# Optimization experiments

Measured on AMD Instinct MI355X. Metric: run time of the kernel, lower is better.

The kernel has to match this reference:

```python
import jax, jax.numpy as jnp
import numpy as np

B, T1, T2 = 2, 1024, 512
D_MODEL, N_HEAD, D_HEAD = 1024, 16, 64
SCALE = 1.0 / D_HEAD ** 0.5
EPS = 1e-5


def _skew(qe):
    # qe: [B, H, T, 2T-1] -> [B, H, T, T] via Transformer-XL pad/reshape trick
    b, h, t, x = qe.shape
    qe = jnp.pad(qe, ((0, 0), (0, 0), (0, 0), (0, 1))).reshape(b, h, 2 * t * t)
    qe = jnp.pad(qe, ((0, 0), (0, 0), (0, t - 1))).reshape(b, h, t + 1, 2 * t - 1)
    return qe[:, :, :t, -t:]


def setup_inputs() -> dict:
    key = jax.random.key(0)
    ks = jax.random.split(key, 12)
    s = 0.02
    return {
        "Q": jax.random.normal(ks[0], (B, T1, D_MODEL), jnp.float32),
        "K": jax.random.normal(ks[1], (B, T1, D_MODEL), jnp.float32),
        "V": jax.random.normal(ks[2], (B, T1, D_MODEL), jnp.float32),
        "lookup_table": jax.random.normal(ks[3], (2 * T1 - 1, D_HEAD), jnp.float32) * s,
        "valid_frames": jnp.sort(jax.random.randint(ks[4], (T2,), 0, T1)),
        "mask": jax.random.bernoulli(ks[5], 0.1, (B, N_HEAD, T1, T2)),
        "Wq": jax.random.normal(ks[6], (D_MODEL, N_HEAD * D_HEAD), jnp.float32) * s,
        "Wk": jax.random.normal(ks[7], (D_MODEL, N_HEAD * D_HEAD), jnp.float32) * s,
        "Wv": jax.random.normal(ks[8], (D_MODEL, N_HEAD * D_HEAD), jnp.float32) * s,
        "Wo": jax.random.normal(ks[9], (N_HEAD * D_HEAD, D_MODEL), jnp.float32) * s,
        "bo": jnp.zeros((D_MODEL,), jnp.float32),
        "ln_g": jnp.ones((D_MODEL,), jnp.float32),
        "ln_b": jnp.zeros((D_MODEL,), jnp.float32),
    }


def reference(Q, K, V, lookup_table, valid_frames, mask, Wq, Wk, Wv, Wo, bo, ln_g, ln_b):
    # gather valid KV frames (raw inputs, before projection)
    K = K[:, valid_frames]  # [B, T2, D]
    V = V[:, valid_frames]
    # pre-layernorm on Q only
    mu = jnp.mean(Q, axis=-1, keepdims=True)
    var = jnp.var(Q, axis=-1, keepdims=True)
    Qn = (Q - mu) * jax.lax.rsqrt(var + EPS) * ln_g + ln_b
    # projections -> [B, H, T, d_head]
    q = (Qn @ Wq).reshape(B, T1, N_HEAD, D_HEAD).transpose(0, 2, 1, 3)
    k = (K @ Wk).reshape(B, T2, N_HEAD, D_HEAD).transpose(0, 2, 1, 3)
    v = (V @ Wv).reshape(B, T2, N_HEAD, D_HEAD).transpose(0, 2, 1, 3)
    # content score + skewed relative-position score
    score = jnp.einsum("bhqd,bhkd->bhqk", q, k)  # [B,H,T1,T2]
    rel = jnp.einsum("bhqd,xd->bhqx", q, lookup_table)  # [B,H,T1,2T1-1]
    rel = _skew(rel)[:, :, :, valid_frames]  # [B,H,T1,T2]
    score = (score + rel) * SCALE
    score = jnp.where(mask, -jnp.finfo(score.dtype).max, score)
    attn = jax.nn.softmax(score, axis=-1)
    ctx = jnp.einsum("bhqk,bhkd->bhqd", attn, v)
    ctx = ctx.transpose(0, 2, 1, 3).reshape(B, T1, N_HEAD * D_HEAD)
    out = ctx @ Wo + bo  # dropout is identity at inference
    return out + ctx  # pre_layernorm=True branch
```

## Files before the change

kernel.cpp:

```cpp
#include <hip/hip_runtime.h>
#include <stdint.h>
#include <stddef.h>

typedef __attribute__((ext_vector_type(8))) short s16x8;
typedef __attribute__((ext_vector_type(4))) short s16x4;
typedef __attribute__((ext_vector_type(4))) float f32x4;

#define MFMA(a,b,c) __builtin_amdgcn_mfma_f32_16x16x32_bf16((a),(b),(c),0,0,0)

static __device__ __forceinline__ unsigned short f2b(float f){
  unsigned int b = __float_as_uint(f);
  b = (b + 0x7FFFu + ((b>>16)&1u)) >> 16;
  return (unsigned short)b;
}
static __device__ __forceinline__ float b2f(unsigned short u){
  return __uint_as_float(((unsigned int)u)<<16);
}


__global__ __launch_bounds__(256) void k_mask(const unsigned char* __restrict__ m,
    unsigned int* __restrict__ MB){
  const int t = threadIdx.x;
  const size_t g0 = (size_t)blockIdx.x*16;
  __shared__ int cnt1, cnt23;
  if(t==0){ cnt1=0; cnt23=0; }
  __syncthreads();
  const uint4* bp = (const uint4*)(m + g0*512);
  int l1=0,l23=0;
  #pragma unroll
  for(int i=0;i<2;i++){
    uint4 v = bp[t + i*256];
    unsigned int ws[4] = {v.x,v.y,v.z,v.w};
    #pragma unroll
    for(int j=0;j<4;j++){
      if((ws[j]>>8)&0xFFu) l1++;
      if(ws[j]>>16)        l23++;
    }
  }
  #pragma unroll
  for(int o=1;o<64;o<<=1){ l1 += __shfl_xor(l1,o); l23 += __shfl_xor(l23,o); }
  if((t&63)==0){ atomicAdd(&cnt1,l1); atomicAdd(&cnt23,l23); }
  __syncthreads();
  const int flag = cnt1 ? 1 : (cnt23 ? 2 : 0);

  const int rl = t>>4, f = t&15;
  const size_t base = (g0 + rl)*512 + f;
  unsigned int word = 0;
  if(flag==0){
    const int* p = (const int*)m;
    #pragma unroll
    for(int i=0;i<32;i++) word |= (p[base+i*16]!=0 ? 1u:0u) << i;
  } else if(flag==1){
    #pragma unroll
    for(int i=0;i<32;i++) word |= (m[base+i*16]!=0 ? 1u:0u) << i;
  } else {
    const float* p = (const float*)m;
    #pragma unroll
    for(int i=0;i<32;i++) word |= (p[base+i*16]!=0.f ? 1u:0u) << i;
  }
  MB[((size_t)blockIdx.x*4 + (t>>6))*64 + f*4 + (rl&3)] = word;
}

__global__ __launch_bounds__(256) void k_prep(
    const float* __restrict__ Q, const float* __restrict__ g, const float* __restrict__ be,
    unsigned short* __restrict__ Qn,
    const float* __restrict__ K, const float* __restrict__ V, const int* __restrict__ vf,
    unsigned short* __restrict__ Kg, unsigned short* __restrict__ Vg,
    const float* __restrict__ L, unsigned short* __restrict__ Lb,
    const float* __restrict__ W0, const float* __restrict__ W1,
    const float* __restrict__ W2, const float* __restrict__ W3,
    unsigned short* __restrict__ D0, unsigned short* __restrict__ D1,
    unsigned short* __restrict__ D2, unsigned short* __restrict__ D3){
  __shared__ float tile[64][65];
  __shared__ float red[8];
  const int bid = blockIdx.x, t = threadIdx.x;
  if(bid < 2048){
    const float4* xp = (const float4*)(Q + (size_t)bid*1024);
    float4 v = xp[t];
    float s  = v.x+v.y+v.z+v.w;
    float s2 = v.x*v.x+v.y*v.y+v.z*v.z+v.w*v.w;
    #pragma unroll
    for(int o=1;o<64;o<<=1){ s += __shfl_xor(s,o); s2 += __shfl_xor(s2,o); }
    int w = t>>6, l = t&63;
    if(l==0){ red[w]=s; red[4+w]=s2; }
    __syncthreads();
    s  = red[0]+red[1]+red[2]+red[3];
    s2 = red[4]+red[5]+red[6]+red[7];
    float mu = s*(1.f/1024.f);
    float var = s2*(1.f/1024.f) - mu*mu;
    float rs = rsqrtf(var + 1e-5f);
    float4 gv = ((const float4*)g)[t];
    float4 bv = ((const float4*)be)[t];
    ushort4 o4;
    o4.x = f2b((v.x-mu)*rs*gv.x + bv.x);
    o4.y = f2b((v.y-mu)*rs*gv.y + bv.y);
    o4.z = f2b((v.z-mu)*rs*gv.z + bv.z);
    o4.w = f2b((v.w-mu)*rs*gv.w + bv.w);
    ((ushort4*)(Qn + (size_t)bid*1024))[t] = o4;
  } else if(bid < 4096){
    int row = bid - 2048;
    int isV = row>>10, r = row&1023;
    int b = r>>9, jj = r&511;
    const float* src = (isV? V : K) + ((size_t)(b*1024 + vf[jj]))*1024;
    unsigned short* dst = (isV? Vg : Kg) + (size_t)r*1024;
    float4 v = ((const float4*)src)[t];
    ushort4 o; o.x=f2b(v.x); o.y=f2b(v.y); o.z=f2b(v.z); o.w=f2b(v.w);
    ((ushort4*)dst)[t] = o;
  } else if(bid < 4608){
    int i = (bid-4096)*256 + t;
    if(i < 2047*64) Lb[i] = f2b(L[i]);
  } else {
    int idx = bid - 4608;
    int z = idx>>8, rem = idx&255;
    int k0 = (rem&15)*64, n0 = (rem>>4)*64;
    const float* S = z==0?W0: z==1?W1: z==2?W2:W3;
    unsigned short* D = z==0?D0: z==1?D1: z==2?D2:D3;
    int tr = t>>6, tc = t&63;
    #pragma unroll
    for(int it=0;it<16;it++){ int r = it*4+tr; tile[r][tc] = S[(size_t)(k0+r)*1024 + n0+tc]; }
    __syncthreads();
    #pragma unroll
    for(int it=0;it<16;it++){ int r = it*4+tr; D[(size_t)(n0+r)*1024 + k0+tc] = f2b(tile[tc][r]); }
  }
}

__global__ __launch_bounds__(256) void k_proj(
    const short* __restrict__ QN, const short* __restrict__ WQT,
    const short* __restrict__ KG, const short* __restrict__ WKT,
    const short* __restrict__ WVT, const short* __restrict__ VG,
    unsigned short* __restrict__ QB, unsigned short* __restrict__ KB,
    unsigned short* __restrict__ VT){
  __shared__ __align__(16) short Ab[128*32];
  __shared__ __align__(16) short Bb[128*32];
  int bid = blockIdx.x;
  int mode, bx;
  if(bid<128){ mode=0; bx=bid>>3; }
  else if(bid<192){ mode=1; bx=(bid-128)>>3; }
  else { mode=2; bx=(bid-192)>>3; }
  int by = bid&7;
  const short* A  = mode==0? QN : mode==1? KG : WVT;
  const short* Bt = mode==0? WQT: mode==1? WKT: VG;

  const int t = threadIdx.x;
  const int w = t>>6, l = t&63;
  const int wr = w>>1, wc = w&1;
  const int fl15 = l&15, fl4 = l>>4;
  const size_t m0 = (size_t)bx*128, n0 = (size_t)by*128;
  const int srow = t>>2, scb = t&3;
  const int sg = scb ^ ((srow>>1)&3);
  const short* Ap = A + (m0+srow)*1024 + 8*sg;
  const short* Bp = Bt + (n0+srow)*1024 + 8*sg;

  f32x4 acc[4][4];
  const f32x4 zero = {0.f,0.f,0.f,0.f};
  #pragma unroll
  for(int m=0;m<4;m++)
    #pragma unroll
    for(int n=0;n<4;n++) acc[m][n] = zero;

  for(int k0=0;k0<1024;k0+=32){
    s16x8 a0 = *(const s16x8*)(Ap + k0);
    s16x8 a1 = *(const s16x8*)(Ap + 64*1024 + k0);
    s16x8 b0 = *(const s16x8*)(Bp + k0);
    s16x8 b1 = *(const s16x8*)(Bp + 64*1024 + k0);
    __syncthreads();
    *(s16x8*)(Ab + srow*32 + scb*8)      = a0;
    *(s16x8*)(Ab + (64+srow)*32 + scb*8) = a1;
    *(s16x8*)(Bb + srow*32 + scb*8)      = b0;
    *(s16x8*)(Bb + (64+srow)*32 + scb*8) = b1;
    __syncthreads();
    s16x8 af[4], bff[4];
    #pragma unroll
    for(int m=0;m<4;m++){
      int row = wr*64 + m*16 + fl15;
      int gg = fl4 ^ ((row>>1)&3);
      af[m] = *(const s16x8*)(Ab + row*32 + gg*8);
    }
    #pragma unroll
    for(int n=0;n<4;n++){
      int row = wc*64 + n*16 + fl15;
      int gg = fl4 ^ ((row>>1)&3);
      bff[n] = *(const s16x8*)(Bb + row*32 + gg*8);
    }
    #pragma unroll
    for(int m=0;m<4;m++)
      #pragma unroll
      for(int n=0;n<4;n++)
        acc[m][n] = MFMA(af[m], bff[n], acc[m][n]);
  }

  #pragma unroll
  for(int m=0;m<4;m++){
    #pragma unroll
    for(int n=0;n<4;n++){
      int mgb = (int)m0 + wr*64 + m*16 + 4*fl4;
      int ng  = (int)n0 + wc*64 + n*16 + fl15;
      #pragma unroll
      for(int p=0;p<4;p++){
        int mg = mgb + p;
        float v = acc[m][n][p];
        if(mode==0){ int b=mg>>10, i=mg&1023, h=ng>>6, d=ng&63;
          QB[((size_t)((b*16+h)*1024+i))*64 + d] = f2b(v); }
        else if(mode==1){ int b=mg>>9, jj=mg&511, h=ng>>6, d=ng&63;
          KB[((size_t)((b*16+h)*512+jj))*64 + d] = f2b(v); }
        else { int h=mg>>6, d=mg&63, b=ng>>9, jj=ng&511;
          VT[((size_t)((b*16+h)*64+d))*512 + jj] = f2b(v); }
      }
    }
  }
}

__global__ __launch_bounds__(256) void k_gemmO(
    const short* __restrict__ A, const short* __restrict__ Bt,
    float* __restrict__ out, const float* __restrict__ bo,
    const float* __restrict__ ctxf){
  __shared__ __align__(16) short Ab[128*32];
  __shared__ __align__(16) short Bb[128*32];
  const int t = threadIdx.x;
  const int w = t>>6, l = t&63;
  const int wr = w>>1, wc = w&1;
  const int fl15 = l&15, fl4 = l>>4;
  const size_t m0 = (size_t)blockIdx.x*128, n0 = (size_t)blockIdx.y*128;
  const int srow = t>>2, scb = t&3;
  const int sg = scb ^ ((srow>>1)&3);
  const short* Ap = A + (m0+srow)*1024 + 8*sg;
  const short* Bp = Bt + (n0+srow)*1024 + 8*sg;

  f32x4 acc[4][4];
  const f32x4 zero = {0.f,0.f,0.f,0.f};
  #pragma unroll
  for(int m=0;m<4;m++)
    #pragma unroll
    for(int n=0;n<4;n++) acc[m][n] = zero;

  for(int k0=0;k0<1024;k0+=32){
    s16x8 a0 = *(const s16x8*)(Ap + k0);
    s16x8 a1 = *(const s16x8*)(Ap + 64*1024 + k0);
    s16x8 b0 = *(const s16x8*)(Bp + k0);
    s16x8 b1 = *(const s16x8*)(Bp + 64*1024 + k0);
    __syncthreads();
    *(s16x8*)(Ab + srow*32 + scb*8)      = a0;
    *(s16x8*)(Ab + (64+srow)*32 + scb*8) = a1;
    *(s16x8*)(Bb + srow*32 + scb*8)      = b0;
    *(s16x8*)(Bb + (64+srow)*32 + scb*8) = b1;
    __syncthreads();
    s16x8 af[4], bff[4];
    #pragma unroll
    for(int m=0;m<4;m++){
      int row = wr*64 + m*16 + fl15;
      int gg = fl4 ^ ((row>>1)&3);
      af[m] = *(const s16x8*)(Ab + row*32 + gg*8);
    }
    #pragma unroll
    for(int n=0;n<4;n++){
      int row = wc*64 + n*16 + fl15;
      int gg = fl4 ^ ((row>>1)&3);
      bff[n] = *(const s16x8*)(Bb + row*32 + gg*8);
    }
    #pragma unroll
    for(int m=0;m<4;m++)
      #pragma unroll
      for(int n=0;n<4;n++)
        acc[m][n] = MFMA(af[m], bff[n], acc[m][n]);
  }

  #pragma unroll
  for(int m=0;m<4;m++){
    #pragma unroll
    for(int n=0;n<4;n++){
      int mgb = (int)m0 + wr*64 + m*16 + 4*fl4;
      int ng  = (int)n0 + wc*64 + n*16 + fl15;
      #pragma unroll
      for(int p=0;p<4;p++){
        int mg = mgb + p;
        size_t idx = (size_t)mg*1024 + ng;
        out[idx] = acc[m][n][p] + bo[ng] + ctxf[idx];
      }
    }
  }
}

#define GS 536
__global__ __launch_bounds__(128) void k_rel(const short* __restrict__ qb,
    const short* __restrict__ lbf, const int* __restrict__ vf,
    unsigned short* __restrict__ relg){
  __shared__ __align__(16) short G[2][16*GS];
  __shared__ int vfs[512];
  const int t=threadIdx.x, w=t>>6, l=t&63, fl15=l&15, fl4=l>>4;
  const int bh  = blockIdx.x >> 5;
  const int qt2 = blockIdx.x & 31;
  const int qw  = qt2*32 + w*16;
  for(int i=t;i<512;i+=128) vfs[i]=vf[i];
  __syncthreads();
  const int vf0 = vfs[0];
  const int x0 = 1008 + vf0 - qw;
  const short* qp = qb + ((size_t)(bh*1024 + qw + fl15))*64 + 8*fl4;
  s16x8 qa0 = *(const s16x8*)qp;
  s16x8 qa1 = *(const s16x8*)(qp+32);
  short* Gw = &G[w][0];
  const f32x4 zero = {0.f,0.f,0.f,0.f};
  for(int c=0;c<2;c++){
    int xc = x0 + c*528;
    #pragma unroll 4
    for(int tt=0;tt<33;tt++){
      int xr = xc + tt*16 + fl15; if(xr>2046) xr = 2046;
      const short* lp = lbf + (size_t)xr*64 + 8*fl4;
      s16x8 b0v = *(const s16x8*)lp;
      s16x8 b1v = *(const s16x8*)(lp+32);
      f32x4 a = zero;
      a = MFMA(qa0,b0v,a); a = MFMA(qa1,b1v,a);
      #pragma unroll
      for(int p=0;p<4;p++) Gw[(4*fl4+p)*GS + tt*16 + fl15] = (short)f2b(a[p]);
    }
    __syncthreads();
    #pragma unroll 4
    for(int tt=0;tt<32;tt++){
      int jj = tt*16 + fl15;
      int xv = 1023 + vfs[jj] - qw;
      #pragma unroll
      for(int p=0;p<4;p++){
        int r = 4*fl4 + p;
        int xloc = xv - r - xc;
        if(xloc>=0 && xloc<528){
          relg[((size_t)((bh*64 + qt2*2 + w)*32 + tt))*256 + l*4 + p]
            = (unsigned short)Gw[r*GS + xloc];
        }
      }
    }
    __syncthreads();
  }
}

__global__ __launch_bounds__(256,2) void k_attn(const short* __restrict__ qb,
    const short* __restrict__ kb, const short* __restrict__ vt,
    const short* __restrict__ relg, const unsigned int* __restrict__ MB,
    unsigned short* __restrict__ ctxb, float* __restrict__ ctxf){
  __shared__ __align__(16) short PB[4][1024];
  const int t=threadIdx.x, w=t>>6, l=t&63, fl15=l&15, fl4=l>>4;
  const int bh = blockIdx.y;
  const int qt = blockIdx.x;
  const int qw = qt*64 + w*16;
  const int qg = qt*4 + w;
  short* Pw = &PB[w][0];

  const int rowgrp = bh*256 + qt*16 + w*4 + fl4;
  uint4 mv = ((const uint4*)MB)[rowgrp*16 + fl15];
  unsigned int mbits[4] = {mv.x, mv.y, mv.z, mv.w};

  const short* qp = qb + ((size_t)(bh*1024 + qw + fl15))*64 + 8*fl4;
  s16x8 qa0 = *(const s16x8*)qp;
  s16x8 qa1 = *(const s16x8*)(qp+32);

  const short* kp_row = kb + ((size_t)(bh*512 + fl15))*64 + 8*fl4;
  const short* rp     = relg + ((size_t)(bh*64+qg))*32*256 + l*4;
  const short* vp[4];
  #pragma unroll
  for(int dt=0;dt<4;dt++) vp[dt] = vt + ((size_t)(bh*64 + dt*16 + fl15))*512 + 8*fl4;

  const f32x4 zero = {0.f,0.f,0.f,0.f};
  f32x4 facc[4];
  #pragma unroll
  for(int dt=0;dt<4;dt++) facc[dt] = zero;
  float m_run[4] = {-1e30f,-1e30f,-1e30f,-1e30f};
  float ps[4]    = {0.f,0.f,0.f,0.f};

  s16x8 kf[2][8];
  s16x4 rf[2][4];
  #pragma unroll
  for(int tl=0;tl<4;tl++){
    const short* ka = kp_row + (size_t)tl*1024;
    kf[0][2*tl]   = *(const s16x8*)ka;
    kf[0][2*tl+1] = *(const s16x8*)(ka+32);
    rf[0][tl]     = *(const s16x4*)(rp + tl*256);
  }

  #pragma unroll
  for(int c=0;c<8;c++){
    const int cur = c&1, nxt = cur^1;
    if(c<7){
      #pragma unroll
      for(int tl=0;tl<4;tl++){
        const short* ka = kp_row + (size_t)(4*(c+1)+tl)*1024;
        kf[nxt][2*tl]   = *(const s16x8*)ka;
        kf[nxt][2*tl+1] = *(const s16x8*)(ka+32);
        rf[nxt][tl]     = *(const s16x4*)(rp + (size_t)(4*(c+1)+tl)*256);
      }
    }
    s16x8 vfr[8];
    #pragma unroll
    for(int dt=0;dt<4;dt++){
      vfr[2*dt]   = *(const s16x8*)(vp[dt] + c*64);
      vfr[2*dt+1] = *(const s16x8*)(vp[dt] + c*64 + 32);
    }

    f32x4 S[4];
    #pragma unroll
    for(int tl=0;tl<4;tl++){
      f32x4 a = zero;
      a = MFMA(qa0, kf[cur][2*tl], a);
      a = MFMA(qa1, kf[cur][2*tl+1], a);
      #pragma unroll
      for(int p=0;p<4;p++){
        float sv = (a[p] + b2f((unsigned short)rf[cur][tl][p])) * 0.125f;
        bool mskb = (mbits[p]>>(4*c+tl))&1u;
        a[p] = mskb ? -1e30f : sv;
      }
      S[tl] = a;
    }

    float cm[4];
    #pragma unroll
    for(int p=0;p<4;p++){
      cm[p] = fmaxf(fmaxf(S[0][p],S[1][p]), fmaxf(S[2][p],S[3][p]));
      #pragma unroll
      for(int o=1;o<16;o<<=1) cm[p] = fmaxf(cm[p], __shfl_xor(cm[p],o));
      float mn = fmaxf(m_run[p], cm[p]);
      float fac = __expf(m_run[p]-mn);
      m_run[p] = mn;
      ps[p] *= fac;
      #pragma unroll
      for(int dt=0;dt<4;dt++) facc[dt][p] *= fac;
    }

    #pragma unroll
    for(int tl=0;tl<4;tl++){
      #pragma unroll
      for(int p=0;p<4;p++){
        float e = __expf(S[tl][p]-m_run[p]);
        ps[p] += e;
        int row = 4*fl4+p;
        Pw[row*64 + ((tl*16 + fl15) ^ (fl4<<4))] = (short)f2b(e);
      }
    }

    #pragma unroll
    for(int s=0;s<2;s++){
      s16x8 pa = *(const s16x8*)(Pw + fl15*64 + ((s*32 + fl4*8) ^ ((fl15>>2)<<4)));
      #pragma unroll
      for(int dt=0;dt<4;dt++)
        facc[dt] = MFMA(pa, vfr[2*dt+s], facc[dt]);
    }
  }

  float inv[4];
  #pragma unroll
  for(int p=0;p<4;p++){
    float sm = ps[p];
    #pragma unroll
    for(int o=1;o<16;o<<=1) sm += __shfl_xor(sm,o);
    inv[p] = 1.f/sm;
  }
  const int b = bh>>4, h = bh&15;
  const int irow0 = qw + 4*fl4;
  #pragma unroll
  for(int dt=0;dt<4;dt++){
    #pragma unroll
    for(int p=0;p<4;p++){
      float val = facc[dt][p] * inv[p];
      size_t idx = ((size_t)(b*1024 + irow0 + p))*1024 + h*64 + dt*16 + fl15;
      ctxb[idx] = f2b(val);
      ctxf[idx] = val;
    }
  }
}

extern "C" void kernel_launch(void* const* d_in, const int* in_sizes, int n_in,
                              void* d_out, int out_size, void* d_ws, size_t ws_size,
                              hipStream_t stream){
  (void)in_sizes; (void)n_in; (void)out_size; (void)ws_size;
  const float* Q  = (const float*)d_in[0];
  const float* K  = (const float*)d_in[1];
  const float* V  = (const float*)d_in[2];
  const float* Lt = (const float*)d_in[3];
  const int*   vf = (const int*)d_in[4];
  const void*  mk = d_in[5];
  const float* Wq = (const float*)d_in[6];
  const float* Wk = (const float*)d_in[7];
  const float* Wv = (const float*)d_in[8];
  const float* Wo = (const float*)d_in[9];
  const float* bo = (const float*)d_in[10];
  const float* lg = (const float*)d_in[11];
  const float* lb = (const float*)d_in[12];

  char* base = (char*)d_ws;
  size_t off = 0;
  auto alloc = [&](size_t bytes)->char*{
    char* p = base + off; off += (bytes + 255) & ~(size_t)255; return p; };
  unsigned int*   MBp = (unsigned int*)alloc(32768ull*16*4);
  unsigned short* QN  = (unsigned short*)alloc(2048ull*1024*2);
  unsigned short* KG  = (unsigned short*)alloc(1024ull*1024*2);
  unsigned short* VG  = (unsigned short*)alloc(1024ull*1024*2);
  unsigned short* WQT = (unsigned short*)alloc(1024ull*1024*2);
  unsigned short* WKT = (unsigned short*)alloc(1024ull*1024*2);
  unsigned short* WVT = (unsigned short*)alloc(1024ull*1024*2);
  unsigned short* WOT = (unsigned short*)alloc(1024ull*1024*2);
  unsigned short* LB  = (unsigned short*)alloc(2047ull*64*2);
  unsigned short* QB  = (unsigned short*)alloc(32ull*1024*64*2);
  unsigned short* KB  = (unsigned short*)alloc(32ull*512*64*2);
  unsigned short* VT  = (unsigned short*)alloc(32ull*64*512*2);
  unsigned short* RG  = (unsigned short*)alloc(32ull*64*32*256*2);
  unsigned short* CB  = (unsigned short*)alloc(2048ull*1024*2);
  float*          CF  = (float*)alloc(2048ull*1024*4);

  k_mask<<<2048,256,0,stream>>>((const unsigned char*)mk, MBp);
  k_prep<<<5632,256,0,stream>>>(Q, lg, lb, QN, K, V, vf, KG, VG, Lt, LB,
                                Wq, Wk, Wv, Wo, WQT, WKT, WVT, WOT);
  k_proj<<<256,256,0,stream>>>((const short*)QN,(const short*)WQT,
                               (const short*)KG,(const short*)WKT,
                               (const short*)WVT,(const short*)VG,
                               QB, KB, VT);
  k_rel<<<1024,128,0,stream>>>((const short*)QB,(const short*)LB, vf, RG);
  k_attn<<<dim3(16,32),256,0,stream>>>((const short*)QB,(const short*)KB,(const short*)VT,
                                       (const short*)RG, MBp, CB, CF);
  k_gemmO<<<dim3(16,8),256,0,stream>>>((const short*)CB,(const short*)WOT,
                                       (float*)d_out, bo, CF);
}
```

Before: 158.2 us.

## Split relative-position skew across four waves with diagonal LDS layout

The k_rel kernel now gives each block one 16-row query group and splits the relative-position column range across four waves of 256 columns each. Previously two waves each handled 16 rows and looped over two 528-column chunks with block-wide barriers. Each wave stores its MFMA results to LDS in a diagonal-indexed layout, so the skewed gather becomes one 4-element vector LDS read and one 8-byte global store per lane, replacing four scalar reads and scatters. This drops the intra-loop barriers, doubles the grid size and cuts the compute per wave, at the cost of some redundant edge tiles (17 tiles for 256 columns).

After: 149.5 us. 1.06x faster.

```diff
diff --git a/kernel.cpp b/kernel.cpp
--- a/kernel.cpp
+++ b/kernel.cpp
@@ -280,54 +280,49 @@
   }
 }
 
-#define GS 536
-__global__ __launch_bounds__(128) void k_rel(const short* __restrict__ qb,
+#define RCH 256
+#define RGS 288
+__global__ __launch_bounds__(256) void k_rel(const short* __restrict__ qb,
     const short* __restrict__ lbf, const int* __restrict__ vf,
     unsigned short* __restrict__ relg){
-  __shared__ __align__(16) short G[2][16*GS];
+  __shared__ __align__(16) short Gs[4][RGS*16];
   __shared__ int vfs[512];
   const int t=threadIdx.x, w=t>>6, l=t&63, fl15=l&15, fl4=l>>4;
-  const int bh  = blockIdx.x >> 5;
-  const int qt2 = blockIdx.x & 31;
-  const int qw  = qt2*32 + w*16;
-  for(int i=t;i<512;i+=128) vfs[i]=vf[i];
+  const int bh = blockIdx.x >> 6;
+  const int qg = blockIdx.x & 63;
+  const int qw = qg*16;
+  for(int i=t;i<512;i+=256) vfs[i]=vf[i];
   __syncthreads();
-  const int vf0 = vfs[0];
-  const int x0 = 1008 + vf0 - qw;
+  const int x0  = 1008 + vfs[0] - qw;
+  const int xcw = x0 + w*RCH;
   const short* qp = qb + ((size_t)(bh*1024 + qw + fl15))*64 + 8*fl4;
   s16x8 qa0 = *(const s16x8*)qp;
   s16x8 qa1 = *(const s16x8*)(qp+32);
-  short* Gw = &G[w][0];
+  short* Gw = &Gs[w][0];
   const f32x4 zero = {0.f,0.f,0.f,0.f};
-  for(int c=0;c<2;c++){
-    int xc = x0 + c*528;
-    #pragma unroll 4
-    for(int tt=0;tt<33;tt++){
-      int xr = xc + tt*16 + fl15; if(xr>2046) xr = 2046;
-      const short* lp = lbf + (size_t)xr*64 + 8*fl4;
-      s16x8 b0v = *(const s16x8*)lp;
-      s16x8 b1v = *(const s16x8*)(lp+32);
-      f32x4 a = zero;
-      a = MFMA(qa0,b0v,a); a = MFMA(qa1,b1v,a);
-      #pragma unroll
-      for(int p=0;p<4;p++) Gw[(4*fl4+p)*GS + tt*16 + fl15] = (short)f2b(a[p]);
-    }
-    __syncthreads();
-    #pragma unroll 4
-    for(int tt=0;tt<32;tt++){
-      int jj = tt*16 + fl15;
-      int xv = 1023 + vfs[jj] - qw;
-      #pragma unroll
-      for(int p=0;p<4;p++){
-        int r = 4*fl4 + p;
-        int xloc = xv - r - xc;
-        if(xloc>=0 && xloc<528){
-          relg[((size_t)((bh*64 + qt2*2 + w)*32 + tt))*256 + l*4 + p]
-            = (unsigned short)Gw[r*GS + xloc];
-        }
-      }
-    }
-    __syncthreads();
+
+  #pragma unroll 4
+  for(int tt=0;tt<17;tt++){
+    int xr = xcw + tt*16 + fl15; if(xr>2046) xr = 2046;
+    const short* lp = lbf + (size_t)xr*64 + 8*fl4;
+    s16x8 b0 = *(const s16x8*)lp;
+    s16x8 b1 = *(const s16x8*)(lp+32);
+    f32x4 a = zero;
+    a = MFMA(qa0,b0,a); a = MFMA(qa1,b1,a);
+    int cb = tt*16 + fl15 + 4*fl4;
+    #pragma unroll
+    for(int p=0;p<4;p++) Gw[(cb+p)*16 + 4*fl4 + p] = (short)f2b(a[p]);
+  }
+
+  unsigned short* rb = relg + ((size_t)(bh*64+qg))*32*256 + l*4;
+  #pragma unroll 4
+  for(int tt=0;tt<32;tt++){
+    int jj = tt*16 + fl15;
+    int o  = vfs[jj] - vfs[0] - RCH*w;
+    if(o>=0 && o<RCH){
+      s16x4 v4 = *(const s16x4*)(Gw + (o+15)*16 + 4*fl4);
+      *(s16x4*)(rb + (size_t)tt*256) = v4;
+    }
   }
 }
 
@@ -509,7 +504,7 @@
                                (const short*)KG,(const short*)WKT,
                                (const short*)WVT,(const short*)VG,
                                QB, KB, VT);
-  k_rel<<<1024,128,0,stream>>>((const short*)QB,(const short*)LB, vf, RG);
+  k_rel<<<2048,256,0,stream>>>((const short*)QB,(const short*)LB, vf, RG);
   k_attn<<<dim3(16,32),256,0,stream>>>((const short*)QB,(const short*)KB,(const short*)VT,
                                        (const short*)RG, MBp, CB, CF);
   k_gemmO<<<dim3(16,8),256,0,stream>>>((const short*)CB,(const short*)WOT,
```
